# Optimization experiments

Measured on AMD Instinct MI355X. Metric: run time of the kernel, lower is better.

## Reference

```python
import jax, jax.numpy as jnp
import numpy as np

K = 16          # k_neighbours
BIG = 1e9       # distance penalty for masked senders


def setup_inputs() -> dict:
    key = jax.random.key(0)
    ks = jax.random.split(key, 8)
    B, N, F, H, FO = 64, 512, 64, 128, 64
    nodes = jax.random.normal(ks[0], (B, N, F), jnp.float32)
    mask = jax.random.randint(ks[1], (B, N), 0, 2, jnp.int32)

    def w(k_, sh):
        return jax.random.normal(k_, sh, jnp.float32) * (1.0 / np.sqrt(sh[0]).astype(np.float32))

    We1 = w(ks[2], (2 * F, H)); be1 = jnp.zeros((H,), jnp.float32)
    We2 = w(ks[3], (H, H));     be2 = jnp.zeros((H,), jnp.float32)
    Wn1 = w(ks[4], (F + H, H)); bn1 = jnp.zeros((H,), jnp.float32)
    Wn2 = w(ks[5], (H, FO));    bn2 = jnp.zeros((FO,), jnp.float32)
    return dict(nodes=nodes, mask=mask, We1=We1, be1=be1, We2=We2, be2=be2,
                Wn1=Wn1, bn1=bn1, Wn2=Wn2, bn2=bn2)


def reference(nodes, mask, We1, be1, We2, be2, Wn1, bn1, Wn2, bn2):
    # nodes: [B,N,F] ; mask: [B,N] (1 = real node, 0 = padding)
    m = mask.astype(nodes.dtype)                      # [B,N]
    x = nodes * m[..., None]                          # zero padded nodes

    # --- dynamic kNN graph (euclidean_squared + top_k, no self connection) ---
    sq = jnp.sum(x * x, axis=-1)                      # [B,N]
    dist = jnp.abs(sq[:, :, None] + sq[:, None, :]
                   - 2.0 * jnp.einsum('bnf,bmf->bnm', x, x))  # [B,N,N]
    dist = dist + BIG * (1.0 - m)[:, None, :]         # never select masked senders
    _, idx = jax.lax.top_k(-dist, K + 1)              # [B,N,K+1]
    idx = idx[..., 1:]                                # drop self connection -> [B,N,K]

    # --- gather sender features / masks along edges ---
    gathered = jax.vmap(lambda xf, ib: xf[ib])(x, idx)    # [B,N,K,F]
    smask = jax.vmap(lambda mv, ib: mv[ib])(m, idx)       # [B,N,K]
    recv = jnp.broadcast_to(x[:, :, None, :], gathered.shape)
    edges = jnp.concatenate([recv, gathered], axis=-1)    # [B,N,K,2F] ('concat' aggregation)

    # --- edge MLP (gather-compute) ---
    h = jax.nn.relu(edges @ We1 + be1)
    h = jax.nn.relu(h @ We2 + be2)                        # [B,N,K,H]

    # --- masked mean pooling over edges (scatter back to nodes) ---
    emask = m[:, :, None] * smask                         # edge valid iff both endpoints valid
    h = h * emask[..., None]
    cnt = jnp.maximum(jnp.sum(emask, axis=-1, keepdims=True), 1.0)  # [B,N,1]
    pooled = jnp.sum(h, axis=2) / cnt                     # [B,N,H]

    # --- node update MLP ---
    nh = jnp.concatenate([x, pooled], axis=-1)            # [B,N,F+H]
    out = jax.nn.relu(nh @ Wn1 + bn1) @ Wn2 + bn2         # [B,N,FO]
    return out * m[..., None]                             # zero padded nodes in output
```

## Files before the change

### kernel.cpp

```cpp
#include <hip/hip_runtime.h>

#define DI __device__ __forceinline__

typedef __bf16 bf16_t;
typedef __bf16 bf16x4 __attribute__((ext_vector_type(4)));
typedef __bf16 bf16x8 __attribute__((ext_vector_type(8)));
typedef float f32x4 __attribute__((ext_vector_type(4)));
typedef unsigned long long u64;


DI bf16_t f2b(float f) {
  unsigned u = __float_as_uint(f);
  unsigned r = (u + 0x7fffu + ((u >> 16) & 1u)) >> 16;
  return __builtin_bit_cast(bf16_t, (unsigned short)r);
}
DI float b2f(bf16_t h) {
  return __uint_as_float(((unsigned)__builtin_bit_cast(unsigned short, h)) << 16);
}
DI f32x4 zero4() { f32x4 z = {0.f, 0.f, 0.f, 0.f}; return z; }

DI void make_frag2(const float* p, bf16x8* hi, bf16x8* lo) {
  float4 v0 = *(const float4*)p;
  float4 v1 = *(const float4*)(p + 4);
  float vv[8] = {v0.x, v0.y, v0.z, v0.w, v1.x, v1.y, v1.z, v1.w};
#pragma unroll
  for (int j = 0; j < 8; ++j) {
    bf16_t h = f2b(vv[j]);
    (*hi)[j] = h;
    (*lo)[j] = f2b(vv[j] - b2f(h));
  }
}

DI u64 u64min(u64 a, u64 b) { return a < b ? a : b; }
template <int CTRL>
DI u64 dpp_u64(u64 v) {
  int lo = (int)(unsigned)(v & 0xffffffffull);
  int hi = (int)(unsigned)(v >> 32);
  int tlo = __builtin_amdgcn_update_dpp(0, lo, CTRL, 0xF, 0xF, true);
  int thi = __builtin_amdgcn_update_dpp(0, hi, CTRL, 0xF, 0xF, true);
  return (((u64)(unsigned)thi) << 32) | (unsigned)tlo;
}
template <int CTRL>
DI float dpp_f32(float v) {
  int t = __builtin_amdgcn_update_dpp(0, (int)__float_as_uint(v), CTRL, 0xF, 0xF, true);
  return __uint_as_float((unsigned)t);
}
DI u64 rowmin_u64(u64 v) {
  v = u64min(v, dpp_u64<0xB1>(v));
  v = u64min(v, dpp_u64<0x4E>(v));
  v = u64min(v, dpp_u64<0x141>(v));
  v = u64min(v, dpp_u64<0x140>(v));
  return v;
}
DI float rowsum_f32(float v) {
  v += dpp_f32<0xB1>(v);
  v += dpp_f32<0x4E>(v);
  v += dpp_f32<0x141>(v);
  v += dpp_f32<0x140>(v);
  return v;
}
DI void bitonic16(u64* a) {
#pragma unroll
  for (int k = 2; k <= 16; k <<= 1)
#pragma unroll
    for (int j = k >> 1; j > 0; j >>= 1)
#pragma unroll
      for (int i = 0; i < 16; ++i) {
        const int l = i ^ j;
        if (l > i) {
          const bool up = ((i & k) == 0);
          const bool sw = up ? (a[i] > a[l]) : (a[i] < a[l]);
          const u64 t0 = a[i], t1 = a[l];
          a[i] = sw ? t1 : t0;
          a[l] = sw ? t0 : t1;
        }
      }
}
DI void sorted_insert16(u64* a, u64 k) {
  u64 na[16];
#pragma unroll
  for (int p = 0; p < 16; ++p) {
    const bool cur_gt = (a[p] > k);
    const bool prv_le = (p == 0) ? true : (a[p - 1] <= k);
    na[p] = !cur_gt ? a[p] : (prv_le ? k : a[p - 1]);
  }
#pragma unroll
  for (int p = 0; p < 16; ++p) a[p] = na[p];
}

__global__ void __launch_bounds__(256) kfuse(const float* __restrict__ nodes,
    const int* __restrict__ mask,
    const float* __restrict__ We1, const float* __restrict__ We2,
    const float* __restrict__ Wn1, const float* __restrict__ Wn2,
    bf16_t* __restrict__ xhi, bf16_t* __restrict__ xlo,
    float* __restrict__ sq, int* __restrict__ vlist, int* __restrict__ vcnt,
    bf16_t* __restrict__ W1p, bf16_t* __restrict__ W2p,
    bf16_t* __restrict__ Wn1p, bf16_t* __restrict__ Wn2p) {
  const int blk = blockIdx.x, t = threadIdx.x;
  __shared__ int cnts[8];
  __shared__ int basep[8];

  if (blk < 512) {
    const int b = blk >> 3, n0 = (blk & 7) * 64;
#pragma unroll
    for (int i = 0; i < 4; ++i) {
      const int idx = t + 256 * i;
      const int gi = b * 512 + n0 + (idx >> 4);
      const int fo = (idx & 15) * 4;
      const float fm = (float)mask[gi];
      const size_t ro = (size_t)gi * 64;
      float4 v = *(const float4*)(nodes + ro + fo);
      v.x *= fm; v.y *= fm; v.z *= fm; v.w *= fm;
      float vv[4] = {v.x, v.y, v.z, v.w};
      bf16x4 hh, ll;
#pragma unroll
      for (int k = 0; k < 4; ++k) {
        bf16_t hi = f2b(vv[k]);
        hh[k] = hi;
        ll[k] = f2b(vv[k] - b2f(hi));
      }
      *(bf16x4*)(xhi + ro + fo) = hh;
      *(bf16x4*)(xlo + ro + fo) = ll;
      float s = v.x * v.x + v.y * v.y + v.z * v.z + v.w * v.w;
      s = rowsum_f32(s);
      if ((t & 15) == 0) sq[gi] = s;
    }
  } else if (blk < 576) {
    const int b = blk - 512, lane = t & 63, w = t >> 6;
    unsigned long long bal[2]; int flag[2];
#pragma unroll
    for (int h = 0; h < 2; ++h) {
      flag[h] = (mask[b * 512 + h * 256 + t] != 0);
      bal[h] = __ballot(flag[h]);
      if (lane == 0) cnts[h * 4 + w] = __popcll(bal[h]);
    }
    __syncthreads();
    if (t == 0) {
      int a = 0;
      for (int c = 0; c < 8; ++c) { basep[c] = a; a += cnts[c]; }
      vcnt[b] = a;
    }
    __syncthreads();
#pragma unroll
    for (int h = 0; h < 2; ++h) {
      if (flag[h]) {
        const unsigned long long lt = (lane == 0) ? 0ull : (~0ull >> (64 - lane));
        const int pos = basep[h * 4 + w] + __popcll(bal[h] & lt);
        vlist[b * 512 + pos] = h * 256 + t;
      }
    }
  } else {
    int p = (blk - 576) * 256 + t;
    const float* W; bf16_t* dst; int K, Nn, local, mode;
    if (p < 4096)       { W = We1; dst = W1p;  K = 128; Nn = 128; mode = 0; local = p; }
    else if (p < 8192)  { W = We2; dst = W2p;  K = 128; Nn = 128; mode = 1; local = p - 4096; }
    else if (p < 14336) { W = Wn1; dst = Wn1p; K = 192; Nn = 128; mode = 0; local = p - 8192; }
    else                { W = Wn2; dst = Wn2p; K = 128; Nn = 64;  mode = 1; local = p - 14336; }
    int lane = local & 63;
    int nnt = (Nn >> 4);
    int chunk = local >> 6;
    int nt = chunk % nnt;
    int s = chunk / nnt;
    int n = nt * 16 + (lane & 15);
    int kbase = s * 32 + ((lane >> 4) * 8);
    bf16x8 v;
#pragma unroll
    for (int j = 0; j < 8; ++j) {
      int kp = kbase + j;
      int region = kp / K;
      int kk = kp - region * K;
      float w = W[kk * Nn + n];
      bf16_t hi = f2b(w);
      v[j] = (mode == 1 && region == 1) ? f2b(w - b2f(hi)) : hi;
    }
    *(bf16x8*)(dst + (size_t)local * 8) = v;
  }
}

__global__ void __launch_bounds__(256) kknn(const bf16_t* __restrict__ xhi,
    const bf16_t* __restrict__ xlo,
    const float* __restrict__ sq, const int* __restrict__ vlist,
    const int* __restrict__ vcnt, int* __restrict__ idxg) {
  const int b = blockIdx.x & 63, tile = blockIdx.x >> 6;
  const int nv = vcnt[b];
  if (tile * 16 >= nv) return;
  const int t = threadIdx.x, lane = t & 63, w = t >> 6;
  const int i = lane >> 4, d = lane & 15;
  __shared__ float sqs[512];
  __shared__ int vls[512];
  __shared__ __align__(16) float S[16 * 520];
  for (int k = t; k < 512; k += 256) { sqs[k] = sq[b * 512 + k]; vls[k] = vlist[b * 512 + k]; }
  __syncthreads();

  const size_t xb = (size_t)b * 512 * 64;

  const int aslot = tile * 16 + d;
  const int arow = vls[aslot < nv ? aslot : 0];
  bf16x8 ah[2], al[2];
#pragma unroll
  for (int kh = 0; kh < 2; ++kh) {
    ah[kh] = *(const bf16x8*)(xhi + xb + (size_t)arow * 64 + kh * 32 + i * 8);
    al[kh] = *(const bf16x8*)(xlo + xb + (size_t)arow * 64 + kh * 32 + i * 8);
  }

  const int rslot = tile * 16 + w * 4 + i;
  const bool vrow = (rslot < nv);
  const int nrow = vls[rslot < nv ? rslot : 0];
  const float sqn = sqs[nrow];

  int crs[8];
#pragma unroll
  for (int jj = 0; jj < 8; ++jj) {
    const int c = (w + 4 * jj) * 16 + d;
    crs[jj] = vls[c < nv ? c : 0];
  }

  bf16x8 pbh[4][2], pbl[4][2];
#pragma unroll
  for (int jj = 0; jj < 4; ++jj) {
    if ((w + 4 * jj) * 16 < nv) {
#pragma unroll
      for (int kh = 0; kh < 2; ++kh) {
        pbh[jj][kh] = *(const bf16x8*)(xhi + xb + (size_t)crs[jj] * 64 + kh * 32 + i * 8);
        pbl[jj][kh] = *(const bf16x8*)(xlo + xb + (size_t)crs[jj] * 64 + kh * 32 + i * 8);
      }
    }
  }
#pragma unroll
  for (int jj = 0; jj < 8; ++jj) {
    const int ct = w + 4 * jj;
    if (ct * 16 < nv) {
      const int sl = jj & 3;
      bf16x8 bh[2] = {pbh[sl][0], pbh[sl][1]};
      bf16x8 bl[2] = {pbl[sl][0], pbl[sl][1]};
      if (jj < 4 && (w + 4 * (jj + 4)) * 16 < nv) {
#pragma unroll
        for (int kh = 0; kh < 2; ++kh) {
          pbh[sl][kh] = *(const bf16x8*)(xhi + xb + (size_t)crs[jj + 4] * 64 + kh * 32 + i * 8);
          pbl[sl][kh] = *(const bf16x8*)(xlo + xb + (size_t)crs[jj + 4] * 64 + kh * 32 + i * 8);
        }
      }
      f32x4 acc = zero4();
#pragma unroll
      for (int kh = 0; kh < 2; ++kh) {
        acc = __builtin_amdgcn_mfma_f32_16x16x32_bf16(ah[kh], bh[kh], acc, 0, 0, 0);
        acc = __builtin_amdgcn_mfma_f32_16x16x32_bf16(ah[kh], bl[kh], acc, 0, 0, 0);
        acc = __builtin_amdgcn_mfma_f32_16x16x32_bf16(al[kh], bh[kh], acc, 0, 0, 0);
        acc = __builtin_amdgcn_mfma_f32_16x16x32_bf16(al[kh], bl[kh], acc, 0, 0, 0);
      }
#pragma unroll
      for (int r = 0; r < 4; ++r) S[(i * 4 + r) * 520 + ct * 16 + d] = acc[r];
    }
  }
  __syncthreads();

  const u64 INF64 = ~0ull;
  u64 s1[16];
#pragma unroll
  for (int j = 0; j < 16; ++j) s1[j] = INF64;
#pragma unroll
  for (int j = 0; j < 16; ++j) {
    if (j * 16 < nv) {
      const int c = j * 16 + d;
      const int m = vls[c < nv ? c : 0];
      const float dot = S[(w * 4 + i) * 520 + j * 16 + d];
      const float dd = fabsf(sqn + sqs[m] - 2.f * dot);
      const u64 key = (((u64)__float_as_uint(dd)) << 32) | (unsigned)m;
      const bool ok = (c < nv) && (m != nrow);
      s1[j] = ok ? key : INF64;
    }
  }
  bitonic16(s1);
  for (int j = 16; j * 16 < nv; ++j) {
    const int c = j * 16 + d;
    const int m = vls[c < nv ? c : 0];
    const float dot = S[(w * 4 + i) * 520 + j * 16 + d];
    const float dd = fabsf(sqn + sqs[m] - 2.f * dot);
    const u64 key = (((u64)__float_as_uint(dd)) << 32) | (unsigned)m;
    const bool ok = (c < nv) && (m != nrow);
    sorted_insert16(s1, ok ? key : INF64);
  }

  int res = nrow;
#pragma unroll
  for (int ts = 0; ts < 16; ++ts) {
    const u64 wmin = rowmin_u64(s1[0]);
    if (d == ts) res = (wmin == INF64) ? nrow : (int)(unsigned)(wmin & 0xffffffffull);
    const bool w1 = (wmin != INF64) && (s1[0] == wmin);
#pragma unroll
    for (int k = 0; k < 15; ++k) s1[k] = w1 ? s1[k + 1] : s1[k];
    s1[15] = w1 ? INF64 : s1[15];
  }
  if (vrow) idxg[((size_t)b * 512 + rslot) * 16 + d] = res;
}

__global__ void __launch_bounds__(256, 2) kedge(const bf16_t* __restrict__ xhi,
    const bf16_t* __restrict__ xlo, const int* __restrict__ idxg,
    const int* __restrict__ vlist, const int* __restrict__ vcnt,
    const bf16_t* __restrict__ W1p, const bf16_t* __restrict__ W2p,
    const float* __restrict__ be1, const float* __restrict__ be2,
    float* __restrict__ pooled) {
  __shared__ __align__(16) bf16_t wbuf[32768];
  __shared__ __align__(16) bf16_t hfrag[4][2][1024];
  const int t = threadIdx.x, lane = t & 63, w = t >> 6;
  const int q = lane >> 4, e = lane & 15;
  const int bb = blockIdx.x & 63;
  const int s0 = ((blockIdx.x >> 6) * 4 + w) * 2;

  {
    const uint4* s1 = (const uint4*)W1p;
    const uint4* s2 = (const uint4*)W2p;
    uint4* dst = (uint4*)wbuf;
#pragma unroll
    for (int i = 0; i < 8; ++i) dst[t + 256 * i] = s1[t + 256 * i];
#pragma unroll
    for (int i = 0; i < 8; ++i) dst[2048 + t + 256 * i] = s2[t + 256 * i];
  }
  __syncthreads();

  const int nv = vcnt[bb];
  if (s0 >= nv) return;

  int vl[2], sv[2];
#pragma unroll
  for (int u = 0; u < 2; ++u) {
    const int sl = (s0 + u) < nv ? (s0 + u) : 0;
    vl[u] = vlist[bb * 512 + sl];
    sv[u] = idxg[((size_t)(bb * 512 + sl) << 4) + e];
  }

  bf16x8 af[2][8];
  {
    const size_t rb0 = (size_t)(bb * 512 + vl[0]) << 6;
    const size_t rb1 = (size_t)(bb * 512 + vl[1]) << 6;
    const size_t nb0 = (size_t)(bb * 512 + sv[0]) << 6;
    const size_t nb1 = (size_t)(bb * 512 + sv[1]) << 6;
#pragma unroll
    for (int k = 0; k < 4; ++k) {
      const int off = (k & 1) * 32 + q * 8;
      const bf16_t* pl = (k >> 1) ? xlo : xhi;
      af[0][k]     = *(const bf16x8*)(pl + rb0 + off);
      af[1][k]     = *(const bf16x8*)(pl + rb1 + off);
      af[0][4 + k] = *(const bf16x8*)(pl + nb0 + off);
      af[1][4 + k] = *(const bf16x8*)(pl + nb1 + off);
    }
  }

  for (int base = s0; base < nv; base += 64) {
    const bool act1 = (base + 1) < nv;
    const bool hasnext = (base + 64) < nv;
    const int gid0 = bb * 512 + vl[0];
    const int gid1 = bb * 512 + vl[1];

    int nvl[2] = {vl[0], vl[1]}, nsv[2] = {sv[0], sv[1]};
    if (hasnext) {
#pragma unroll
      for (int u = 0; u < 2; ++u) {
        const int sl = (base + 64 + u) < nv ? (base + 64 + u) : 0;
        nvl[u] = vlist[bb * 512 + sl];
        nsv[u] = idxg[((size_t)(bb * 512 + sl) << 4) + e];
      }
    }

    f32x4 acc[2][8];
#pragma unroll
    for (int u = 0; u < 2; ++u)
#pragma unroll
      for (int nt = 0; nt < 8; ++nt) acc[u][nt] = zero4();

#pragma unroll
    for (int ph = 0; ph < 2; ++ph)
#pragma unroll
      for (int inner = 0; inner < 2; ++inner) {
        const bf16_t* wb = wbuf + (ph * 2 + inner) * 4096;
        const bf16x8 h0 = af[0][ph * 4 + inner];
        const bf16x8 h1 = af[1][ph * 4 + inner];
        const bf16x8 l0 = af[0][ph * 4 + 2 + inner];
        const bf16x8 l1 = af[1][ph * 4 + 2 + inner];
#pragma unroll
        for (int nt = 0; nt < 8; ++nt) {
          const bf16x8 bfv = *(const bf16x8*)(wb + (nt * 64 + lane) * 8);
          acc[0][nt] = __builtin_amdgcn_mfma_f32_16x16x32_bf16(h0, bfv, acc[0][nt], 0, 0, 0);
          acc[0][nt] = __builtin_amdgcn_mfma_f32_16x16x32_bf16(l0, bfv, acc[0][nt], 0, 0, 0);
          acc[1][nt] = __builtin_amdgcn_mfma_f32_16x16x32_bf16(h1, bfv, acc[1][nt], 0, 0, 0);
          acc[1][nt] = __builtin_amdgcn_mfma_f32_16x16x32_bf16(l1, bfv, acc[1][nt], 0, 0, 0);
        }
      }

    bf16x8 naf[2][8];
    if (hasnext) {
      const size_t rb0n = (size_t)(bb * 512 + nvl[0]) << 6;
      const size_t rb1n = (size_t)(bb * 512 + nvl[1]) << 6;
      const size_t nb0n = (size_t)(bb * 512 + nsv[0]) << 6;
      const size_t nb1n = (size_t)(bb * 512 + nsv[1]) << 6;
#pragma unroll
      for (int k = 0; k < 4; ++k) {
        const int off = (k & 1) * 32 + q * 8;
        const bf16_t* pl = (k >> 1) ? xlo : xhi;
        naf[0][k]     = *(const bf16x8*)(pl + rb0n + off);
        naf[1][k]     = *(const bf16x8*)(pl + rb1n + off);
        naf[0][4 + k] = *(const bf16x8*)(pl + nb0n + off);
        naf[1][4 + k] = *(const bf16x8*)(pl + nb1n + off);
      }
    }

    f32x4 acc2[2][8];
#pragma unroll
    for (int u = 0; u < 2; ++u)
#pragma unroll
      for (int nt = 0; nt < 8; ++nt) acc2[u][nt] = zero4();

#pragma unroll
    for (int hh = 0; hh < 2; ++hh) {
#pragma unroll
      for (int u = 0; u < 2; ++u)
#pragma unroll
        for (int nt4 = 0; nt4 < 4; ++nt4) {
          const int nt = hh * 4 + nt4;
          const int cc = nt * 16 + e;
          const float bv = be1[cc];
          const int bse = (((cc >> 5) & 1) * 64 + q * 4 + 16 * ((cc >> 3) & 3)) * 8 + (cc & 7);
#pragma unroll
          for (int r = 0; r < 4; ++r)
            hfrag[w][u][bse + r * 8] = f2b(fmaxf(acc[u][nt][r] + bv, 0.f));
        }
#pragma unroll
      for (int sl = 0; sl < 2; ++sl) {
        const int f = hh * 2 + sl;
        const bf16x8 a20 = *(const bf16x8*)(&hfrag[w][0][(sl * 64 + lane) * 8]);
        const bf16x8 a21 = *(const bf16x8*)(&hfrag[w][1][(sl * 64 + lane) * 8]);
        const bf16_t* wb2 = wbuf + 16384 + f * 4096;
#pragma unroll
        for (int nt = 0; nt < 8; ++nt) {
          const bf16x8 bfv = *(const bf16x8*)(wb2 + (nt * 64 + lane) * 8);
          acc2[0][nt] = __builtin_amdgcn_mfma_f32_16x16x32_bf16(a20, bfv, acc2[0][nt], 0, 0, 0);
          acc2[1][nt] = __builtin_amdgcn_mfma_f32_16x16x32_bf16(a21, bfv, acc2[1][nt], 0, 0, 0);
        }
      }
    }

#pragma unroll
    for (int u = 0; u < 2; ++u) {
      if (u == 0 || act1) {
        const int gid = u ? gid1 : gid0;
#pragma unroll
        for (int nt = 0; nt < 8; ++nt) {
          const float bv = be2[nt * 16 + e];
          float part = 0.f;
#pragma unroll
          for (int r = 0; r < 4; ++r) part += fmaxf(acc2[u][nt][r] + bv, 0.f);
          part += __shfl_xor(part, 16, 64);
          part += __shfl_xor(part, 32, 64);
          if (lane < 16) pooled[(size_t)gid * 128 + nt * 16 + lane] = part * 0.0625f;
        }
      }
    }

    if (hasnext) {
#pragma unroll
      for (int u = 0; u < 2; ++u)
#pragma unroll
        for (int k = 0; k < 8; ++k) af[u][k] = naf[u][k];
      vl[0] = nvl[0]; vl[1] = nvl[1];
      sv[0] = nsv[0]; sv[1] = nsv[1];
    }
  }
}

__global__ void __launch_bounds__(256, 2) knode(const bf16_t* __restrict__ xhi,
    const bf16_t* __restrict__ xlo,
    const float* __restrict__ pooled, const int* __restrict__ mask,
    const bf16_t* __restrict__ Wn1p, const bf16_t* __restrict__ Wn2p,
    const float* __restrict__ bn1, const float* __restrict__ bn2,
    float* __restrict__ out) {
  __shared__ __align__(16) bf16_t wbuf[32768];
  __shared__ __align__(16) bf16_t hfrag[4][1024];
  const int t = threadIdx.x, lane = t & 63, w = t >> 6;
  const int q = lane >> 4, e = lane & 15;
  const int nodebase = (blockIdx.x * 4 + w) * 16;

  {
    const uint4* s1 = (const uint4*)Wn1p;
    const uint4* s2 = (const uint4*)Wn2p;
    uint4* dst = (uint4*)wbuf;
#pragma unroll
    for (int i = 0; i < 12; ++i) dst[t + 256 * i] = s1[t + 256 * i];
#pragma unroll
    for (int i = 0; i < 4; ++i) dst[3072 + t + 256 * i] = s2[t + 256 * i];
  }
  __syncthreads();

  f32x4 acc[8];
#pragma unroll
  for (int nt = 0; nt < 8; ++nt) acc[nt] = zero4();

#pragma unroll
  for (int sr = 0; sr < 6; ++sr) {
    const int col = sr * 32 + q * 8;
    const int node = nodebase + e;
    bf16x8 afh, afl;
    if (sr < 2) {
      afh = *(const bf16x8*)(xhi + (size_t)node * 64 + col);
      afl = *(const bf16x8*)(xlo + (size_t)node * 64 + col);
    } else {
      make_frag2(pooled + (size_t)node * 128 + (col - 64), &afh, &afl);
    }
#pragma unroll
    for (int nt = 0; nt < 8; ++nt) {
      const bf16x8 bfv = *(const bf16x8*)(wbuf + sr * 4096 + (nt * 64 + lane) * 8);
      acc[nt] = __builtin_amdgcn_mfma_f32_16x16x32_bf16(afh, bfv, acc[nt], 0, 0, 0);
      acc[nt] = __builtin_amdgcn_mfma_f32_16x16x32_bf16(afl, bfv, acc[nt], 0, 0, 0);
    }
  }

  f32x4 acc2[4];
#pragma unroll
  for (int nt = 0; nt < 4; ++nt) acc2[nt] = zero4();

#pragma unroll
  for (int hh = 0; hh < 2; ++hh) {
#pragma unroll
    for (int nt4 = 0; nt4 < 4; ++nt4) {
      const int nt = hh * 4 + nt4;
      const int cc = nt * 16 + e;
      const float bv = bn1[cc];
      const int bse = (((cc >> 5) & 1) * 64 + q * 4 + 16 * ((cc >> 3) & 3)) * 8 + (cc & 7);
#pragma unroll
      for (int r = 0; r < 4; ++r)
        hfrag[w][bse + r * 8] = f2b(fmaxf(acc[nt][r] + bv, 0.f));
    }
#pragma unroll
    for (int sl = 0; sl < 2; ++sl) {
      const int f = hh * 2 + sl;
      const bf16x8 a2 = *(const bf16x8*)(&hfrag[w][(sl * 64 + lane) * 8]);
      const bf16_t* wb2 = wbuf + 24576 + f * 2048;
#pragma unroll
      for (int nt = 0; nt < 4; ++nt) {
        const bf16x8 bfv = *(const bf16x8*)(wb2 + (nt * 64 + lane) * 8);
        acc2[nt] = __builtin_amdgcn_mfma_f32_16x16x32_bf16(a2, bfv, acc2[nt], 0, 0, 0);
      }
    }
  }

  int mm[4];
#pragma unroll
  for (int r = 0; r < 4; ++r) mm[r] = mask[nodebase + q * 4 + r];
#pragma unroll
  for (int nt = 0; nt < 4; ++nt) {
    const float bv = bn2[nt * 16 + e];
#pragma unroll
    for (int r = 0; r < 4; ++r) {
      const int node = nodebase + q * 4 + r;
      out[(size_t)node * 64 + nt * 16 + e] = (acc2[nt][r] + bv) * (float)mm[r];
    }
  }
}

extern "C" void kernel_launch(void* const* d_in, const int* in_sizes, int n_in,
                              void* d_out, int out_size, void* d_ws, size_t ws_size,
                              hipStream_t stream) {
  const float* nodes = (const float*)d_in[0];
  const int*   mask  = (const int*)d_in[1];
  const float* We1   = (const float*)d_in[2];
  const float* be1   = (const float*)d_in[3];
  const float* We2   = (const float*)d_in[4];
  const float* be2   = (const float*)d_in[5];
  const float* Wn1   = (const float*)d_in[6];
  const float* bn1   = (const float*)d_in[7];
  const float* Wn2   = (const float*)d_in[8];
  const float* bn2   = (const float*)d_in[9];
  float* out = (float*)d_out;

  char* p = (char*)d_ws;
  auto alloc = [&](size_t bytes) -> char* {
    char* r = p;
    p += (bytes + 255) & ~(size_t)255;
    return r;
  };
  bf16_t* xhi    = (bf16_t*)alloc((size_t)32768 * 64 * 2);
  bf16_t* xlo    = (bf16_t*)alloc((size_t)32768 * 64 * 2);
  float*  sq     = (float*)alloc((size_t)32768 * 4);
  int*    vlist  = (int*)alloc((size_t)32768 * 4);
  int*    vcnt   = (int*)alloc((size_t)64 * 4);
  int*    idxg   = (int*)alloc((size_t)32768 * 16 * 4);
  float*  pooled = (float*)alloc((size_t)32768 * 128 * 4);
  bf16_t* W1p    = (bf16_t*)alloc((size_t)8 * 8 * 64 * 8 * 2);
  bf16_t* W2p    = (bf16_t*)alloc((size_t)8 * 8 * 64 * 8 * 2);
  bf16_t* Wn1p   = (bf16_t*)alloc((size_t)12 * 8 * 64 * 8 * 2);
  bf16_t* Wn2p   = (bf16_t*)alloc((size_t)8 * 4 * 64 * 8 * 2);
  if ((size_t)(p - (char*)d_ws) > ws_size) return;

  kfuse<<<640, 256, 0, stream>>>(nodes, mask, We1, We2, Wn1, Wn2,
                                 xhi, xlo, sq, vlist, vcnt, W1p, W2p, Wn1p, Wn2p);
  kknn<<<2048, 256, 0, stream>>>(xhi, xlo, sq, vlist, vcnt, idxg);
  kedge<<<512, 256, 0, stream>>>(xhi, xlo, idxg, vlist, vcnt, W1p, W2p, be1, be2, pooled);
  knode<<<512, 256, 0, stream>>>(xhi, xlo, pooled, mask, Wn1p, Wn2p, bn1, bn2, out);
}
```

Baseline: 154.3 us.

## Precompute receiver half of edge layer-1 once per node in kNN kernel

The first edge-MLP layer is split algebraically. The receiver-feature product x_recv·We1[:F] is computed once per node by extra blocks appended to the kNN launch and stored in a recvpart buffer. The edge kernel then seeds its accumulators from recvpart and runs MFMAs only over the gathered sender features, which halves layer-1 MFMA work and register-held fragments. The cost is a 16MB fp32 intermediate write and read, plus removal of the next-iteration prefetch of fragments in the edge loop.

```diff
diff --git a/kernel.cpp b/kernel.cpp
--- a/kernel.cpp
+++ b/kernel.cpp
@@ -180,15 +180,54 @@
 __global__ void __launch_bounds__(256) kknn(const bf16_t* __restrict__ xhi,
     const bf16_t* __restrict__ xlo,
     const float* __restrict__ sq, const int* __restrict__ vlist,
-    const int* __restrict__ vcnt, int* __restrict__ idxg) {
+    const int* __restrict__ vcnt, int* __restrict__ idxg,
+    const bf16_t* __restrict__ W1p, float* __restrict__ recvpart) {
+  __shared__ __align__(16) unsigned char smem[37376];
+  const int t = threadIdx.x, lane = t & 63, w = t >> 6;
+  const int i = lane >> 4, d = lane & 15;
+  const int q = i, e = d;
+
+  if (blockIdx.x >= 2048) {
+    const int blk2 = blockIdx.x - 2048;
+    bf16_t* wbuf = (bf16_t*)smem;
+    {
+      const uint4* s1 = (const uint4*)W1p;
+      uint4* dst = (uint4*)wbuf;
+#pragma unroll
+      for (int k = 0; k < 4; ++k) dst[t + 256 * k] = s1[t + 256 * k];
+    }
+    __syncthreads();
+    const int nodebase = (blk2 * 4 + w) * 16;
+    f32x4 acc[8];
+#pragma unroll
+    for (int nt = 0; nt < 8; ++nt) acc[nt] = zero4();
+#pragma unroll
+    for (int inner = 0; inner < 2; ++inner) {
+      const int off = inner * 32 + q * 8;
+      const int node = nodebase + e;
+      const bf16x8 h = *(const bf16x8*)(xhi + (size_t)node * 64 + off);
+      const bf16x8 l = *(const bf16x8*)(xlo + (size_t)node * 64 + off);
+#pragma unroll
+      for (int nt = 0; nt < 8; ++nt) {
+        const bf16x8 bfv = *(const bf16x8*)(wbuf + inner * 4096 + (nt * 64 + lane) * 8);
+        acc[nt] = __builtin_amdgcn_mfma_f32_16x16x32_bf16(h, bfv, acc[nt], 0, 0, 0);
+        acc[nt] = __builtin_amdgcn_mfma_f32_16x16x32_bf16(l, bfv, acc[nt], 0, 0, 0);
+      }
+    }
+#pragma unroll
+    for (int nt = 0; nt < 8; ++nt)
+#pragma unroll
+      for (int r = 0; r < 4; ++r)
+        recvpart[(size_t)(nodebase + q * 4 + r) * 128 + nt * 16 + e] = acc[nt][r];
+    return;
+  }
+
   const int b = blockIdx.x & 63, tile = blockIdx.x >> 6;
   const int nv = vcnt[b];
   if (tile * 16 >= nv) return;
-  const int t = threadIdx.x, lane = t & 63, w = t >> 6;
-  const int i = lane >> 4, d = lane & 15;
-  __shared__ float sqs[512];
-  __shared__ int vls[512];
-  __shared__ __align__(16) float S[16 * 520];
+  float* sqs = (float*)smem;
+  int* vls = (int*)(smem + 2048);
+  float* S = (float*)(smem + 4096);
   for (int k = t; k < 512; k += 256) { sqs[k] = sq[b * 512 + k]; vls[k] = vlist[b * 512 + k]; }
   __syncthreads();
 
@@ -295,12 +334,13 @@
 }
 
 __global__ void __launch_bounds__(256, 2) kedge(const bf16_t* __restrict__ xhi,
-    const bf16_t* __restrict__ xlo, const int* __restrict__ idxg,
-    const int* __restrict__ vlist, const int* __restrict__ vcnt,
+    const bf16_t* __restrict__ xlo, const float* __restrict__ recvpart,
+    const int* __restrict__ idxg, const int* __restrict__ vlist,
+    const int* __restrict__ vcnt,
     const bf16_t* __restrict__ W1p, const bf16_t* __restrict__ W2p,
     const float* __restrict__ be1, const float* __restrict__ be2,
     float* __restrict__ pooled) {
-  __shared__ __align__(16) bf16_t wbuf[32768];
+  __shared__ __align__(16) bf16_t wbuf[24576];
   __shared__ __align__(16) bf16_t hfrag[4][2][1024];
   const int t = threadIdx.x, lane = t & 63, w = t >> 6;
   const int q = lane >> 4, e = lane & 15;
@@ -308,13 +348,13 @@
   const int s0 = ((blockIdx.x >> 6) * 4 + w) * 2;
 
   {
-    const uint4* s1 = (const uint4*)W1p;
+    const uint4* s1 = (const uint4*)(W1p + 8192);
     const uint4* s2 = (const uint4*)W2p;
     uint4* dst = (uint4*)wbuf;
 #pragma unroll
-    for (int i = 0; i < 8; ++i) dst[t + 256 * i] = s1[t + 256 * i];
-#pragma unroll
-    for (int i = 0; i < 8; ++i) dst[2048 + t + 256 * i] = s2[t + 256 * i];
+    for (int i = 0; i < 4; ++i) dst[t + 256 * i] = s1[t + 256 * i];
+#pragma unroll
+    for (int i = 0; i < 8; ++i) dst[1024 + t + 256 * i] = s2[t + 256 * i];
   }
   __syncthreads();
 
@@ -329,78 +369,62 @@
     sv[u] = idxg[((size_t)(bb * 512 + sl) << 4) + e];
   }
 
-  bf16x8 af[2][8];
-  {
-    const size_t rb0 = (size_t)(bb * 512 + vl[0]) << 6;
-    const size_t rb1 = (size_t)(bb * 512 + vl[1]) << 6;
+  for (int base = s0; base < nv; base += 64) {
+    const bool act1 = (base + 1) < nv;
+    const int gid0 = bb * 512 + vl[0];
+    const int gid1 = bb * 512 + vl[1];
     const size_t nb0 = (size_t)(bb * 512 + sv[0]) << 6;
     const size_t nb1 = (size_t)(bb * 512 + sv[1]) << 6;
-#pragma unroll
-    for (int k = 0; k < 4; ++k) {
-      const int off = (k & 1) * 32 + q * 8;
-      const bf16_t* pl = (k >> 1) ? xlo : xhi;
-      af[0][k]     = *(const bf16x8*)(pl + rb0 + off);
-      af[1][k]     = *(const bf16x8*)(pl + rb1 + off);
-      af[0][4 + k] = *(const bf16x8*)(pl + nb0 + off);
-      af[1][4 + k] = *(const bf16x8*)(pl + nb1 + off);
-    }
-  }
-
-  for (int base = s0; base < nv; base += 64) {
-    const bool act1 = (base + 1) < nv;
-    const bool hasnext = (base + 64) < nv;
-    const int gid0 = bb * 512 + vl[0];
-    const int gid1 = bb * 512 + vl[1];
+
+    bf16x8 af[2][4];
+#pragma unroll
+    for (int k = 0; k < 2; ++k) {
+      const int off = k * 32 + q * 8;
+      af[0][k]     = *(const bf16x8*)(xhi + nb0 + off);
+      af[1][k]     = *(const bf16x8*)(xhi + nb1 + off);
+      af[0][2 + k] = *(const bf16x8*)(xlo + nb0 + off);
+      af[1][2 + k] = *(const bf16x8*)(xlo + nb1 + off);
+    }
+
+    f32x4 acc[2][8];
+#pragma unroll
+    for (int u = 0; u < 2; ++u) {
+      const int gid = u ? gid1 : gid0;
+#pragma unroll
+      for (int nt = 0; nt < 8; ++nt) {
+        const float rv = recvpart[(size_t)gid * 128 + nt * 16 + e];
+        f32x4 v = {rv, rv, rv, rv};
+        acc[u][nt] = v;
+      }
+    }
 
     int nvl[2] = {vl[0], vl[1]}, nsv[2] = {sv[0], sv[1]};
-    if (hasnext) {
-#pragma unroll
-      for (int u = 0; u < 2; ++u) {
-        const int sl = (base + 64 + u) < nv ? (base + 64 + u) : 0;
-        nvl[u] = vlist[bb * 512 + sl];
-        nsv[u] = idxg[((size_t)(bb * 512 + sl) << 4) + e];
-      }
-    }
-
-    f32x4 acc[2][8];
-#pragma unroll
-    for (int u = 0; u < 2; ++u)
-#pragma unroll
-      for (int nt = 0; nt < 8; ++nt) acc[u][nt] = zero4();
-
-#pragma unroll
-    for (int ph = 0; ph < 2; ++ph)
-#pragma unroll
-      for (int inner = 0; inner < 2; ++inner) {
-        const bf16_t* wb = wbuf + (ph * 2 + inner) * 4096;
-        const bf16x8 h0 = af[0][ph * 4 + inner];
-        const bf16x8 h1 = af[1][ph * 4 + inner];
-        const bf16x8 l0 = af[0][ph * 4 + 2 + inner];
-        const bf16x8 l1 = af[1][ph * 4 + 2 + inner];
-#pragma unroll
-        for (int nt = 0; nt < 8; ++nt) {
-          const bf16x8 bfv = *(const bf16x8*)(wb + (nt * 64 + lane) * 8);
-          acc[0][nt] = __builtin_amdgcn_mfma_f32_16x16x32_bf16(h0, bfv, acc[0][nt], 0, 0, 0);
-          acc[0][nt] = __builtin_amdgcn_mfma_f32_16x16x32_bf16(l0, bfv, acc[0][nt], 0, 0, 0);
-          acc[1][nt] = __builtin_amdgcn_mfma_f32_16x16x32_bf16(h1, bfv, acc[1][nt], 0, 0, 0);
-          acc[1][nt] = __builtin_amdgcn_mfma_f32_16x16x32_bf16(l1, bfv, acc[1][nt], 0, 0, 0);
+    {
+      const int nbs = base + 64;
+      if (nbs < nv) {
+#pragma unroll
+        for (int u = 0; u < 2; ++u) {
+          const int sl = (nbs + u) < nv ? (nbs + u) : 0;
+          nvl[u] = vlist[bb * 512 + sl];
+          nsv[u] = idxg[((size_t)(bb * 512 + sl) << 4) + e];
         }
       }
-
-    bf16x8 naf[2][8];
-    if (hasnext) {
-      const size_t rb0n = (size_t)(bb * 512 + nvl[0]) << 6;
-      const size_t rb1n = (size_t)(bb * 512 + nvl[1]) << 6;
-      const size_t nb0n = (size_t)(bb * 512 + nsv[0]) << 6;
-      const size_t nb1n = (size_t)(bb * 512 + nsv[1]) << 6;
-#pragma unroll
-      for (int k = 0; k < 4; ++k) {
-        const int off = (k & 1) * 32 + q * 8;
-        const bf16_t* pl = (k >> 1) ? xlo : xhi;
-        naf[0][k]     = *(const bf16x8*)(pl + rb0n + off);
-        naf[1][k]     = *(const bf16x8*)(pl + rb1n + off);
-        naf[0][4 + k] = *(const bf16x8*)(pl + nb0n + off);
-        naf[1][4 + k] = *(const bf16x8*)(pl + nb1n + off);
+    }
+
+#pragma unroll
+    for (int inner = 0; inner < 2; ++inner) {
+      const bf16_t* wb = wbuf + inner * 4096;
+      const bf16x8 h0 = af[0][inner];
+      const bf16x8 h1 = af[1][inner];
+      const bf16x8 l0 = af[0][2 + inner];
+      const bf16x8 l1 = af[1][2 + inner];
+#pragma unroll
+      for (int nt = 0; nt < 8; ++nt) {
+        const bf16x8 bfv = *(const bf16x8*)(wb + (nt * 64 + lane) * 8);
+        acc[0][nt] = __builtin_amdgcn_mfma_f32_16x16x32_bf16(h0, bfv, acc[0][nt], 0, 0, 0);
+        acc[0][nt] = __builtin_amdgcn_mfma_f32_16x16x32_bf16(l0, bfv, acc[0][nt], 0, 0, 0);
+        acc[1][nt] = __builtin_amdgcn_mfma_f32_16x16x32_bf16(h1, bfv, acc[1][nt], 0, 0, 0);
+        acc[1][nt] = __builtin_amdgcn_mfma_f32_16x16x32_bf16(l1, bfv, acc[1][nt], 0, 0, 0);
       }
     }
 
@@ -429,7 +453,7 @@
         const int f = hh * 2 + sl;
         const bf16x8 a20 = *(const bf16x8*)(&hfrag[w][0][(sl * 64 + lane) * 8]);
         const bf16x8 a21 = *(const bf16x8*)(&hfrag[w][1][(sl * 64 + lane) * 8]);
-        const bf16_t* wb2 = wbuf + 16384 + f * 4096;
+        const bf16_t* wb2 = wbuf + 8192 + f * 4096;
 #pragma unroll
         for (int nt = 0; nt < 8; ++nt) {
           const bf16x8 bfv = *(const bf16x8*)(wb2 + (nt * 64 + lane) * 8);
@@ -456,14 +480,8 @@
       }
     }
 
-    if (hasnext) {
-#pragma unroll
-      for (int u = 0; u < 2; ++u)
-#pragma unroll
-        for (int k = 0; k < 8; ++k) af[u][k] = naf[u][k];
-      vl[0] = nvl[0]; vl[1] = nvl[1];
-      sv[0] = nsv[0]; sv[1] = nsv[1];
-    }
+    vl[0] = nvl[0]; vl[1] = nvl[1];
+    sv[0] = nsv[0]; sv[1] = nsv[1];
   }
 }
 
@@ -577,22 +595,24 @@
     p += (bytes + 255) & ~(size_t)255;
     return r;
   };
-  bf16_t* xhi    = (bf16_t*)alloc((size_t)32768 * 64 * 2);
-  bf16_t* xlo    = (bf16_t*)alloc((size_t)32768 * 64 * 2);
-  float*  sq     = (float*)alloc((size_t)32768 * 4);
-  int*    vlist  = (int*)alloc((size_t)32768 * 4);
-  int*    vcnt   = (int*)alloc((size_t)64 * 4);
-  int*    idxg   = (int*)alloc((size_t)32768 * 16 * 4);
-  float*  pooled = (float*)alloc((size_t)32768 * 128 * 4);
-  bf16_t* W1p    = (bf16_t*)alloc((size_t)8 * 8 * 64 * 8 * 2);
-  bf16_t* W2p    = (bf16_t*)alloc((size_t)8 * 8 * 64 * 8 * 2);
-  bf16_t* Wn1p   = (bf16_t*)alloc((size_t)12 * 8 * 64 * 8 * 2);
-  bf16_t* Wn2p   = (bf16_t*)alloc((size_t)8 * 4 * 64 * 8 * 2);
+  bf16_t* xhi      = (bf16_t*)alloc((size_t)32768 * 64 * 2);
+  bf16_t* xlo      = (bf16_t*)alloc((size_t)32768 * 64 * 2);
+  float*  sq       = (float*)alloc((size_t)32768 * 4);
+  int*    vlist    = (int*)alloc((size_t)32768 * 4);
+  int*    vcnt     = (int*)alloc((size_t)64 * 4);
+  int*    idxg     = (int*)alloc((size_t)32768 * 16 * 4);
+  float*  pooled   = (float*)alloc((size_t)32768 * 128 * 4);
+  float*  recvpart = (float*)alloc((size_t)32768 * 128 * 4);
+  bf16_t* W1p      = (bf16_t*)alloc((size_t)8 * 8 * 64 * 8 * 2);
+  bf16_t* W2p      = (bf16_t*)alloc((size_t)8 * 8 * 64 * 8 * 2);
+  bf16_t* Wn1p     = (bf16_t*)alloc((size_t)12 * 8 * 64 * 8 * 2);
+  bf16_t* Wn2p     = (bf16_t*)alloc((size_t)8 * 4 * 64 * 8 * 2);
   if ((size_t)(p - (char*)d_ws) > ws_size) return;
 
   kfuse<<<640, 256, 0, stream>>>(nodes, mask, We1, We2, Wn1, Wn2,
                                  xhi, xlo, sq, vlist, vcnt, W1p, W2p, Wn1p, Wn2p);
-  kknn<<<2048, 256, 0, stream>>>(xhi, xlo, sq, vlist, vcnt, idxg);
-  kedge<<<512, 256, 0, stream>>>(xhi, xlo, idxg, vlist, vcnt, W1p, W2p, be1, be2, pooled);
+  kknn<<<2560, 256, 0, stream>>>(xhi, xlo, sq, vlist, vcnt, idxg, W1p, recvpart);
+  kedge<<<512, 256, 0, stream>>>(xhi, xlo, recvpart, idxg, vlist, vcnt,
+                                 W1p, W2p, be1, be2, pooled);
   knode<<<512, 256, 0, stream>>>(xhi, xlo, pooled, mask, Wn1p, Wn2p, bn1, bn2, out);
 }
```

New measurement: 151.6 us. Within noise of the previous version (-1.8%).
